# Optimization experiments

Hardware: AMD Instinct MI355X
Metric: run time of the kernel (lower is better)

Reference implementation:

```python
import jax, jax.numpy as jnp
import numpy as np
from jax.scipy.linalg import solve_triangular

L_SUB = 16          # subarray length (init arg L)
DL = 0.05           # diagonal loading factor


def setup_inputs() -> dict:
    key = jax.random.key(0)
    k0, k1, k2 = jax.random.split(key, 3)
    B, C, NS, NZ, NX = 2, 128, 1024, 256, 128
    rf = jax.random.normal(k0, (B, C, NS), jnp.float32)
    t0 = jnp.zeros((B,), jnp.float32)
    d_tx = jax.random.uniform(k1, (B, NZ, NX), dtype=jnp.float32)
    d_rx = jax.random.uniform(k2, (C, NZ, NX), dtype=jnp.float32)
    fs = jnp.float32((NS - 1) / 2.0)   # keeps sample positions in [0, NS-1]
    f0 = jnp.float32(5.0)              # unused by forward (kept for signature parity)
    c0 = jnp.float32(1.0)
    apod = jnp.ones((C,), jnp.float32) # unused by forward
    return dict(rf=rf, t0=t0, d_tx=d_tx, d_rx=d_rx, fs=fs, f0=f0, c0=c0, apod=apod)


def _aligned_signals(rf, t0, d_tx, d_rx, fs, c0):
    """Bilinear (1-D linear) resample of rf at per-pixel delays.
    Equivalent to torch grid_sample(mode='bilinear', padding_mode='border',
    align_corners=True) where the grid x-coord is samples*2/(NS-1)-1."""
    B, C, NS = rf.shape
    _, NZ, NX = d_tx.shape
    # samples: [B, C, NZ, NX] fractional sample index into rf
    samples = fs * ((d_tx[:, None, :, :] + d_rx[None, :, :, :]) / c0
                    + t0[:, None, None, None])
    pos = jnp.clip(samples, 0.0, NS - 1.0)          # border padding
    i0 = jnp.floor(pos).astype(jnp.int32)
    i1 = jnp.minimum(i0 + 1, NS - 1)
    frac = pos - i0.astype(pos.dtype)
    sig = rf.reshape(B * C, NS)
    i0f = i0.reshape(B * C, NZ * NX)
    i1f = i1.reshape(B * C, NZ * NX)
    v0 = jnp.take_along_axis(sig, i0f, axis=1).reshape(B, C, NZ, NX)
    v1 = jnp.take_along_axis(sig, i1f, axis=1).reshape(B, C, NZ, NX)
    return v0 * (1.0 - frac) + v1 * frac


def reference(rf, t0, d_tx, d_rx, fs, f0, c0, apod):
    B, C, NS = rf.shape
    _, NZ, NX = d_tx.shape
    M = C - L_SUB + 1  # number of subarrays (113)
    aligned = _aligned_signals(rf, t0, d_tx, d_rx, fs, c0)  # [B, C, NZ, NX]
    # per-pixel channel vectors: [P, C], P = B*NZ*NX
    xf = aligned.transpose(0, 2, 3, 1).reshape(-1, C)
    # subarray gather: S[p, m, l] = xf[p, m + l]  -> [P, M, L]
    idx = jnp.arange(M)[:, None] + jnp.arange(L_SUB)[None, :]
    S = xf[:, idx]
    # avg_pool1d(kernel=M, stride=1) over channels == mean over subarray axis
    x = S.mean(axis=1)                                  # [P, L]
    # spatially-smoothed covariance: R = S^T S / M, symmetrized
    R = jnp.einsum('pml,pmk->plk', S, S) / M
    R = 0.5 * (R + R.transpose(0, 2, 1))
    # diagonal loading: R += dl * (trace/L) * I
    delta = jnp.trace(R, axis1=-2, axis2=-1) / L_SUB    # [P]
    R = R + (DL * delta)[:, None, None] * jnp.eye(L_SUB, dtype=R.dtype)
    # Cholesky solve R u = 1
    Lc = jnp.linalg.cholesky(R)
    rhs = jnp.ones((R.shape[0], L_SUB, 1), R.dtype)
    y1 = solve_triangular(Lc, rhs, lower=True)
    u = solve_triangular(Lc, y1, lower=True, trans=1)[..., 0]  # [P, L]
    # MVDR weights (steering a = ones) and beamformed output
    denom = jnp.sum(u, axis=-1, keepdims=True) + 1e-10
    w = u / denom
    y = jnp.sum(w * x, axis=-1)                         # [P]
    return y.reshape(B, NZ, NX)
```

## Files before the change

### kernel.cpp

```cpp
#include <hip/hip_runtime.h>


namespace {

constexpr int kB  = 2;
constexpr int kC  = 128;
constexpr int kNS = 1024;
constexpr int kNZ = 256;
constexpr int kNX = 128;
constexpr int kZX = kNZ * kNX;
constexpr int kNPIX = kB * kZX;
constexpr int kChunk = 8;
constexpr int kTPB = 128;

__device__ __host__ constexpr int tri(int l, int k) {
  return l * 16 - (l * (l - 1)) / 2 + (k - l);
}

typedef __attribute__((address_space(1))) const void gconst_t;
typedef __attribute__((address_space(3))) void ldsv_t;

__device__ __forceinline__ void g2l16(const float* g, float* l) {
  __builtin_amdgcn_global_load_lds((gconst_t*)g, (ldsv_t*)l, 16, 0, 0);
}

__device__ __forceinline__ void stage_chunk(const float* __restrict__ gsrc,
                                            float* lbase, int woff, int lane) {
#pragma unroll
  for (int i = 0; i < 16; ++i)
    g2l16(gsrc + i * 512 + woff + lane * 4, lbase + i * 512 + woff);
}

template <int PH, bool HEAD>
__device__ __forceinline__ void chunk_compute(
    const float (&rows)[kChunk][kNS], int cbase,
    const float* __restrict__ drx_px, float kk, float base,
    float (&F)[16], float (&win)[16], float (&head)[16], float& Sall) {
  float drx[kChunk];
#pragma unroll
  for (int r = 0; r < kChunk; ++r)
    drx[r] = drx_px[(size_t)(cbase + r) * kZX];

#pragma unroll
  for (int r = 0; r < kChunk; ++r) {
    const int t = PH + r;
    float pos = fmaf(kk, drx[r], base);
    pos = fminf(fmaxf(pos, 0.0f), 1023.0f);
    int i0 = (int)pos;
    float frac = pos - (float)i0;
    int i1 = min(i0 + 1, kNS - 1);
    float v0 = rows[r][i0];
    float v1 = rows[r][i1];
    float v = fmaf(frac, v1 - v0, v0);
    Sall += v;
    F[0] = fmaf(v, v, F[0]);
    if constexpr (HEAD) {
#pragma unroll
      for (int d = 1; d <= t; ++d) F[d] = fmaf(v, win[t - d], F[d]);
      head[t] = v;
    } else {
#pragma unroll
      for (int d = 1; d < 16; ++d) F[d] = fmaf(v, win[(t - d) & 15], F[d]);
    }
    win[t] = v;
  }
}

__global__ __launch_bounds__(kTPB, 1) void mvb_window_kernel(
    const float* __restrict__ rf, const float* __restrict__ t0,
    const float* __restrict__ d_tx, const float* __restrict__ d_rx,
    const float* __restrict__ fs_p, const float* __restrict__ c0_p,
    float* __restrict__ ws) {
  __shared__ float tile[2][kChunk][kNS];

  const int tid = threadIdx.x;
  const int lane = tid & 63;
  const int wave = tid >> 6;
  const int woff = wave * 256;
  const int z = blockIdx.x & (kNZ - 1);
  const int b = blockIdx.x >> 8;
  const int x = tid;
  const int pix = (int)((size_t)b * kZX + z * kNX + x);

  const float fs = fs_p[0];
  const float c0 = c0_p[0];
  const float kk = fs / c0;
  const float base =
      fs * (d_tx[(size_t)b * kZX + z * kNX + x] / c0 + t0[b]);

  const float* rfb = rf + (size_t)b * kC * kNS;
  const float* drx_px = d_rx + (size_t)z * kNX + x;

  float F[16], win[16], head[16];
  float Sall = 0.0f;
#pragma unroll
  for (int i = 0; i < 16; ++i) F[i] = 0.0f;

  stage_chunk(rfb, &tile[0][0][0], woff, lane);
  __syncthreads();

  stage_chunk(rfb + 1 * kChunk * kNS, &tile[1][0][0], woff, lane);
  chunk_compute<0, true>(tile[0], 0, drx_px, kk, base, F, win, head, Sall);
  __syncthreads();

  stage_chunk(rfb + 2 * kChunk * kNS, &tile[0][0][0], woff, lane);
  chunk_compute<8, true>(tile[1], 8, drx_px, kk, base, F, win, head, Sall);
  __syncthreads();

  for (int g = 0; g < 7; ++g) {
    const int q0 = 2 * g + 2;
    stage_chunk(rfb + (size_t)(q0 + 1) * kChunk * kNS, &tile[1][0][0], woff,
                lane);
    chunk_compute<0, false>(tile[0], q0 * kChunk, drx_px, kk, base, F, win,
                            head, Sall);
    __syncthreads();

    if (q0 + 2 < 16)
      stage_chunk(rfb + (size_t)(q0 + 2) * kChunk * kNS, &tile[0][0][0], woff,
                  lane);
    chunk_compute<8, false>(tile[1], (q0 + 1) * kChunk, drx_px, kk, base, F,
                            win, head, Sall);
    __syncthreads();
  }

#pragma unroll
  for (int i = 0; i < 16; ++i) ws[(size_t)i * kNPIX + pix] = F[i];
#pragma unroll
  for (int i = 0; i < 16; ++i) ws[(size_t)(16 + i) * kNPIX + pix] = win[i];
#pragma unroll
  for (int i = 0; i < 16; ++i) ws[(size_t)(32 + i) * kNPIX + pix] = head[i];
  ws[(size_t)48 * kNPIX + pix] = Sall;
}

__global__ __launch_bounds__(256, 1) void mvb_solve_kernel(
    const float* __restrict__ ws, float* __restrict__ out) {
  const int pix = blockIdx.x * 256 + threadIdx.x;

  float F[16], win[16], head[16];
#pragma unroll
  for (int i = 0; i < 16; ++i) F[i] = ws[(size_t)i * kNPIX + pix];
#pragma unroll
  for (int i = 0; i < 16; ++i) win[i] = ws[(size_t)(16 + i) * kNPIX + pix];
#pragma unroll
  for (int i = 0; i < 16; ++i) head[i] = ws[(size_t)(32 + i) * kNPIX + pix];
  const float Sall = ws[(size_t)48 * kNPIX + pix];

  float Ru[136];
#pragma unroll
  for (int d = 0; d < 16; ++d) {
    float t0s = 0.0f;
#pragma unroll
    for (int i = d + 1; i < 16; ++i) t0s = fmaf(win[i - d], win[i], t0s);
    Ru[tri(0, d)] = F[d] - t0s;
#pragma unroll
    for (int l = 1; l < 16 - d; ++l)
      Ru[tri(l, l + d)] = Ru[tri(l - 1, l - 1 + d)] -
                          head[l - 1] * head[l - 1 + d] +
                          win[l] * win[l + d];
  }

  float tr = 0.0f;
#pragma unroll
  for (int l = 0; l < 16; ++l) tr += Ru[tri(l, l)];
  const float dl = tr * (0.05f / 16.0f);
#pragma unroll
  for (int l = 0; l < 16; ++l) Ru[tri(l, l)] += dl;

  float X[16];
  {
    float s = Sall;
#pragma unroll
    for (int i = 1; i < 16; ++i) s -= win[i];
    X[0] = s;
#pragma unroll
    for (int l = 1; l < 16; ++l) X[l] = X[l - 1] - head[l - 1] + win[l];
  }

  float inv[16];
#pragma unroll
  for (int j = 0; j < 16; ++j) {
    float d = Ru[tri(j, j)];
#pragma unroll
    for (int p = 0; p < j; ++p) d = fmaf(-Ru[tri(p, j)], Ru[tri(p, j)], d);
    float Ljj = sqrtf(d);
    inv[j] = 1.0f / Ljj;
    Ru[tri(j, j)] = Ljj;
#pragma unroll
    for (int i = j + 1; i < 16; ++i) {
      float s = Ru[tri(j, i)];
#pragma unroll
      for (int p = 0; p < j; ++p) s = fmaf(-Ru[tri(p, i)], Ru[tri(p, j)], s);
      Ru[tri(j, i)] = s * inv[j];
    }
  }

  float yv[16];
#pragma unroll
  for (int i = 0; i < 16; ++i) {
    float s = 1.0f;
#pragma unroll
    for (int j = 0; j < i; ++j) s = fmaf(-Ru[tri(j, i)], yv[j], s);
    yv[i] = s * inv[i];
  }
  float u[16];
#pragma unroll
  for (int i = 15; i >= 0; --i) {
    float s = yv[i];
#pragma unroll
    for (int j = i + 1; j < 16; ++j) s = fmaf(-Ru[tri(i, j)], u[j], s);
    u[i] = s * inv[i];
  }

  float su = 0.0f, dot = 0.0f;
#pragma unroll
  for (int i = 0; i < 16; ++i) {
    su += u[i];
    dot = fmaf(u[i], X[i], dot);
  }
  out[pix] = dot / (113.0f * su + 1e-10f);
}

}

extern "C" void kernel_launch(void* const* d_in, const int* in_sizes, int n_in,
                              void* d_out, int out_size, void* d_ws,
                              size_t ws_size, hipStream_t stream) {
  const float* rf   = (const float*)d_in[0];
  const float* t0   = (const float*)d_in[1];
  const float* d_tx = (const float*)d_in[2];
  const float* d_rx = (const float*)d_in[3];
  const float* fs   = (const float*)d_in[4];
  const float* c0   = (const float*)d_in[6];
  float* out = (float*)d_out;
  float* ws  = (float*)d_ws;

  hipLaunchKernelGGL(mvb_window_kernel, dim3(kB * kNZ), dim3(kTPB), 0, stream,
                     rf, t0, d_tx, d_rx, fs, c0, ws);
  hipLaunchKernelGGL(mvb_solve_kernel, dim3(kNPIX / 256), dim3(256), 0, stream,
                     ws, out);
}
```

Before: 105.9 us.

## Share staged rf tiles across two rows per block and prefetch d_rx

The window kernel now runs 256 threads per block covering two z rows, so each staged 8-channel rf chunk in LDS serves twice as many pixels and global-to-LDS traffic is halved. The d_rx delay values for the next chunk are loaded into registers alongside the LDS staging, so their latency overlaps compute. The interpolation index is clamped so the two adjacent reads come from one pointer. The solve kernel switches to 64-thread blocks for more blocks across CUs. In exchange the grid is halved to 256 blocks, which lowers parallelism in the window kernel.

```diff
diff --git a/kernel.cpp b/kernel.cpp
--- a/kernel.cpp
+++ b/kernel.cpp
@@ -11,7 +11,8 @@
 constexpr int kZX = kNZ * kNX;
 constexpr int kNPIX = kB * kZX;
 constexpr int kChunk = 8;
-constexpr int kTPB = 128;
+constexpr int kChunkF = kChunk * kNS;
+constexpr int kTPA = 256;
 
 __device__ __host__ constexpr int tri(int l, int k) {
   return l * 16 - (l * (l - 1)) / 2 + (k - l);
@@ -25,32 +26,34 @@
 }
 
 __device__ __forceinline__ void stage_chunk(const float* __restrict__ gsrc,
-                                            float* lbase, int woff, int lane) {
-#pragma unroll
-  for (int i = 0; i < 16; ++i)
-    g2l16(gsrc + i * 512 + woff + lane * 4, lbase + i * 512 + woff);
+                                            float* ldst, int woff, int lane) {
+#pragma unroll
+  for (int i = 0; i < 8; ++i)
+    g2l16(gsrc + woff + i * 256 + lane * 4, ldst + woff + i * 256);
+}
+
+__device__ __forceinline__ void load_drx(const float* __restrict__ drx_px,
+                                         int cbase, float (&d)[kChunk]) {
+#pragma unroll
+  for (int r = 0; r < kChunk; ++r)
+    d[r] = drx_px[(size_t)(cbase + r) * kZX];
 }
 
 template <int PH, bool HEAD>
 __device__ __forceinline__ void chunk_compute(
-    const float (&rows)[kChunk][kNS], int cbase,
-    const float* __restrict__ drx_px, float kk, float base,
+    const float* rows, const float (&drx)[kChunk], float kk, float base,
     float (&F)[16], float (&win)[16], float (&head)[16], float& Sall) {
-  float drx[kChunk];
-#pragma unroll
-  for (int r = 0; r < kChunk; ++r)
-    drx[r] = drx_px[(size_t)(cbase + r) * kZX];
-
 #pragma unroll
   for (int r = 0; r < kChunk; ++r) {
     const int t = PH + r;
     float pos = fmaf(kk, drx[r], base);
     pos = fminf(fmaxf(pos, 0.0f), 1023.0f);
     int i0 = (int)pos;
+    i0 = min(i0, kNS - 2);
     float frac = pos - (float)i0;
-    int i1 = min(i0 + 1, kNS - 1);
-    float v0 = rows[r][i0];
-    float v1 = rows[r][i1];
+    const float* p = rows + r * kNS + i0;
+    float v0 = p[0];
+    float v1 = p[1];
     float v = fmaf(frac, v1 - v0, v0);
     Sall += v;
     F[0] = fmaf(v, v, F[0]);
@@ -66,27 +69,26 @@
   }
 }
 
-__global__ __launch_bounds__(kTPB, 1) void mvb_window_kernel(
+__global__ __launch_bounds__(kTPA, 1) void mvb_window_kernel(
     const float* __restrict__ rf, const float* __restrict__ t0,
     const float* __restrict__ d_tx, const float* __restrict__ d_rx,
     const float* __restrict__ fs_p, const float* __restrict__ c0_p,
     float* __restrict__ ws) {
-  __shared__ float tile[2][kChunk][kNS];
+  __shared__ float tile[2 * kChunkF];
 
   const int tid = threadIdx.x;
   const int lane = tid & 63;
   const int wave = tid >> 6;
-  const int woff = wave * 256;
-  const int z = blockIdx.x & (kNZ - 1);
-  const int b = blockIdx.x >> 8;
-  const int x = tid;
+  const int woff = wave * 2048;
+  const int b = blockIdx.x >> 7;
+  const int z = ((blockIdx.x & 127) << 1) + (tid >> 7);
+  const int x = tid & 127;
   const int pix = (int)((size_t)b * kZX + z * kNX + x);
 
   const float fs = fs_p[0];
   const float c0 = c0_p[0];
   const float kk = fs / c0;
-  const float base =
-      fs * (d_tx[(size_t)b * kZX + z * kNX + x] / c0 + t0[b]);
+  const float base = fs * (d_tx[pix] / c0 + t0[b]);
 
   const float* rfb = rf + (size_t)b * kC * kNS;
   const float* drx_px = d_rx + (size_t)z * kNX + x;
@@ -96,30 +98,35 @@
 #pragma unroll
   for (int i = 0; i < 16; ++i) F[i] = 0.0f;
 
-  stage_chunk(rfb, &tile[0][0][0], woff, lane);
+  float drx0[kChunk], drx1[kChunk];
+
+  stage_chunk(rfb, tile, woff, lane);
+  load_drx(drx_px, 0, drx0);
   __syncthreads();
 
-  stage_chunk(rfb + 1 * kChunk * kNS, &tile[1][0][0], woff, lane);
-  chunk_compute<0, true>(tile[0], 0, drx_px, kk, base, F, win, head, Sall);
+  stage_chunk(rfb + kChunkF, tile + kChunkF, woff, lane);
+  load_drx(drx_px, 8, drx1);
+  chunk_compute<0, true>(tile, drx0, kk, base, F, win, head, Sall);
   __syncthreads();
 
-  stage_chunk(rfb + 2 * kChunk * kNS, &tile[0][0][0], woff, lane);
-  chunk_compute<8, true>(tile[1], 8, drx_px, kk, base, F, win, head, Sall);
+  stage_chunk(rfb + 2 * kChunkF, tile, woff, lane);
+  load_drx(drx_px, 16, drx0);
+  chunk_compute<8, true>(tile + kChunkF, drx1, kk, base, F, win, head, Sall);
   __syncthreads();
 
   for (int g = 0; g < 7; ++g) {
     const int q0 = 2 * g + 2;
-    stage_chunk(rfb + (size_t)(q0 + 1) * kChunk * kNS, &tile[1][0][0], woff,
-                lane);
-    chunk_compute<0, false>(tile[0], q0 * kChunk, drx_px, kk, base, F, win,
-                            head, Sall);
+    stage_chunk(rfb + (size_t)(q0 + 1) * kChunkF, tile + kChunkF, woff, lane);
+    load_drx(drx_px, (q0 + 1) * kChunk, drx1);
+    chunk_compute<0, false>(tile, drx0, kk, base, F, win, head, Sall);
     __syncthreads();
 
-    if (q0 + 2 < 16)
-      stage_chunk(rfb + (size_t)(q0 + 2) * kChunk * kNS, &tile[0][0][0], woff,
-                  lane);
-    chunk_compute<8, false>(tile[1], (q0 + 1) * kChunk, drx_px, kk, base, F,
-                            win, head, Sall);
+    if (q0 + 2 < 16) {
+      stage_chunk(rfb + (size_t)(q0 + 2) * kChunkF, tile, woff, lane);
+      load_drx(drx_px, (q0 + 2) * kChunk, drx0);
+    }
+    chunk_compute<8, false>(tile + kChunkF, drx1, kk, base, F, win, head,
+                            Sall);
     __syncthreads();
   }
 
@@ -132,9 +139,9 @@
   ws[(size_t)48 * kNPIX + pix] = Sall;
 }
 
-__global__ __launch_bounds__(256, 1) void mvb_solve_kernel(
+__global__ __launch_bounds__(64, 1) void mvb_solve_kernel(
     const float* __restrict__ ws, float* __restrict__ out) {
-  const int pix = blockIdx.x * 256 + threadIdx.x;
+  const int pix = blockIdx.x * 64 + threadIdx.x;
 
   float F[16], win[16], head[16];
 #pragma unroll
@@ -234,8 +241,8 @@
   float* out = (float*)d_out;
   float* ws  = (float*)d_ws;
 
-  hipLaunchKernelGGL(mvb_window_kernel, dim3(kB * kNZ), dim3(kTPB), 0, stream,
-                     rf, t0, d_tx, d_rx, fs, c0, ws);
-  hipLaunchKernelGGL(mvb_solve_kernel, dim3(kNPIX / 256), dim3(256), 0, stream,
+  hipLaunchKernelGGL(mvb_window_kernel, dim3(kB * kNZ / 2), dim3(kTPA), 0,
+                     stream, rf, t0, d_tx, d_rx, fs, c0, ws);
+  hipLaunchKernelGGL(mvb_solve_kernel, dim3(kNPIX / 64), dim3(64), 0, stream,
                      ws, out);
 }
```

Result: faster. 100.2 us (-5.4%).
